# Kernel tuning notes

Hardware: AMD Instinct MI355X
Metric: run time of the kernel (lower is better)

The kernel has to match this reference:

```python
import jax, jax.numpy as jnp
import numpy as np

CHUNK_SIZE = 2048
LOCAL_WINDOW = 384
CHUNK_LEN = CHUNK_SIZE - LOCAL_WINDOW  # 1664
N_HEADS = 16
N_KV_HEADS = 4
HEAD_DIM = 128
HIDDEN = 2048
SEQ = 3 * CHUNK_LEN  # 4992
NEG_INF = -1e9


def _cos_sin(positions, dim=HEAD_DIM, base=10000.0):
    inv = 1.0 / (base ** (np.arange(0, dim, 2, dtype=np.float64) / dim))
    freqs = np.outer(np.asarray(positions, np.float64), inv)
    emb = np.concatenate([freqs, freqs], axis=-1)
    return jnp.asarray(np.cos(emb), jnp.float32), jnp.asarray(np.sin(emb), jnp.float32)


def setup_inputs() -> dict:
    key = jax.random.key(0)
    ks = jax.random.split(key, 5)
    hidden_states = jax.random.normal(ks[0], (1, SEQ, HIDDEN), jnp.float32) * 0.02
    position_ids = jnp.arange(SEQ, dtype=jnp.int32)[None, :]
    q_cos, q_sin = _cos_sin(np.arange(SEQ))                 # intra rotary (positions mod chunk_len)
    qc_cos, qc_sin = _cos_sin(np.arange(SEQ) + CHUNK_LEN)   # cross-chunk rotary variant
    k_cos, k_sin = _cos_sin(np.arange(SEQ))                 # key rotary (absolute positions)
    kv_dim = N_KV_HEADS * HEAD_DIM
    Wq = jax.random.normal(ks[1], (N_HEADS * HEAD_DIM, HIDDEN), jnp.float32) * 0.02
    Wk = jax.random.normal(ks[2], (kv_dim, HIDDEN), jnp.float32) * 0.02
    Wv = jax.random.normal(ks[3], (kv_dim, HIDDEN), jnp.float32) * 0.02
    Wo = jax.random.normal(ks[4], (HIDDEN, N_HEADS * HEAD_DIM), jnp.float32) * 0.02
    return dict(hidden_states=hidden_states, position_ids=position_ids,
                q_cos=q_cos, q_sin=q_sin, qc_cos=qc_cos, qc_sin=qc_sin,
                k_cos=k_cos, k_sin=k_sin, Wq=Wq, Wk=Wk, Wv=Wv, Wo=Wo)


def _rotate_half(x):
    x1, x2 = jnp.split(x, 2, axis=-1)
    return jnp.concatenate([-x2, x1], axis=-1)


def _rope(x, cos_t, sin_t, pid):
    # x: [b,h,s,d], pid: [b,s] -> cos/sin [b,1,s,d]
    cos = cos_t[pid][:, None]
    sin = sin_t[pid][:, None]
    return x * cos + _rotate_half(x) * sin


def _attn(q, k, v, causal):
    # flash-attn semantics: scale = head_dim**-0.5, returns output and fp32 LSE [b,h,q]
    scale = q.shape[-1] ** -0.5
    s = jnp.einsum('bhqd,bhkd->bhqk', q, k).astype(jnp.float32) * scale
    if causal:
        L, K = s.shape[-2], s.shape[-1]
        mask = jnp.tril(jnp.ones((L, K), bool))
        s = jnp.where(mask, s, NEG_INF)
    lse = jax.nn.logsumexp(s, axis=-1)
    p = jax.nn.softmax(s, axis=-1).astype(q.dtype)
    out = jnp.einsum('bhqk,bhkd->bhqd', p, v)
    return out, lse


def _merge(parts):
    # LSE-weighted merge of partial attention outputs (weights detached, as in torch)
    outs = jnp.stack([p[0] for p in parts])       # [n,b,h,q,d]
    lses = jnp.stack([p[1] for p in parts])       # [n,b,h,q] fp32
    w = jax.lax.stop_gradient(jax.nn.softmax(lses, axis=0))
    return jnp.sum(outs * w[..., None].astype(outs.dtype), axis=0)


def _forward(hidden_states, position_ids, q_cos, q_sin, qc_cos, qc_sin, k_cos, k_sin, Wq, Wk, Wv, Wo):
    b, s, _ = hidden_states.shape
    q = (hidden_states @ Wq.T).reshape(b, s, N_HEADS, HEAD_DIM).transpose(0, 2, 1, 3)
    k = (hidden_states @ Wk.T).reshape(b, s, N_KV_HEADS, HEAD_DIM).transpose(0, 2, 1, 3)
    v = (hidden_states @ Wv.T).reshape(b, s, N_KV_HEADS, HEAD_DIM).transpose(0, 2, 1, 3)

    k = _rope(k, k_cos, k_sin, position_ids)
    pid = position_ids % CHUNK_LEN

    groups = N_HEADS // N_KV_HEADS
    k = jnp.repeat(k, groups, axis=1)
    v = jnp.repeat(v, groups, axis=1)

    n_chunks = s // CHUNK_LEN
    # chunk 0: intra causal only
    q0 = _rope(q[:, :, :CHUNK_LEN], q_cos, q_sin, pid[:, :CHUNK_LEN])
    out0, _ = _attn(q0, k[:, :, :CHUNK_LEN], v[:, :, :CHUNK_LEN], causal=True)
    outs = [out0]
    for i in range(1, n_chunks):
        b0 = i * CHUNK_LEN
        e = b0 + CHUNK_LEN
        qi = q[:, :, b0:e]
        pid_c = pid[:, b0:e]
        parts = [_attn(_rope(qi, q_cos, q_sin, pid_c), k[:, :, b0:e], v[:, :, b0:e], causal=True),
                 _attn(_rope(qi, qc_cos, qc_sin, pid_c), k[:, :, b0 - CHUNK_LEN:b0], v[:, :, b0 - CHUNK_LEN:b0], causal=False)]
        if b0 - CHUNK_LEN > 0:
            pid_i = jnp.full_like(pid_c, CHUNK_LEN - 1)
            parts.append(_attn(_rope(qi, qc_cos, qc_sin, pid_i), k[:, :, :b0 - CHUNK_LEN], v[:, :, :b0 - CHUNK_LEN], causal=False))
        outs.append(_merge(parts))
    attn_out = jnp.concatenate(outs, axis=2)                      # [b,h,s,d]
    attn_out = attn_out.transpose(0, 2, 1, 3).reshape(b, s, -1)   # [b,s,h*d]
    return attn_out @ Wo.T


def reference(hidden_states, position_ids, q_cos, q_sin, qc_cos, qc_sin, k_cos, k_sin, Wq, Wk, Wv, Wo):
    return _forward(hidden_states, position_ids, q_cos, q_sin, qc_cos, qc_sin, k_cos, k_sin, Wq, Wk, Wv, Wo)
```

## Files before the change

### kernel.cpp

```cpp
#include <hip/hip_runtime.h>

typedef unsigned short u16;
typedef unsigned int u32;
typedef __attribute__((ext_vector_type(8))) __bf16 bf16x8;
typedef __attribute__((ext_vector_type(4))) float f32x4;
typedef __attribute__((ext_vector_type(16))) float f32x16;

#define CLEN 1664
#define SEQL 4992
#define NHEADS 16
#define HD 128
#define HID 2048
#define KVD 512
#define SCALE 0.08838834764831845f
#define SCLOG2E 0.12752615142058843f

__device__ __forceinline__ u16 f2bf(float f) {
  union { float f; u32 u; } v; v.f = f;
  u32 u = v.u;
  return (u16)((u + 0x7FFFu + ((u >> 16) & 1u)) >> 16);
}
__device__ __forceinline__ float bf2f(u16 h) {
  union { u32 u; float f; } v; v.u = (u32)h << 16;
  return v.f;
}
__device__ __forceinline__ f32x4 mfma16(bf16x8 a, bf16x8 b, f32x4 c) {
  return __builtin_amdgcn_mfma_f32_16x16x32_bf16(a, b, c, 0, 0, 0);
}
__device__ __forceinline__ f32x16 mfma32(bf16x8 a, bf16x8 b, f32x16 c) {
  return __builtin_amdgcn_mfma_f32_32x32x16_bf16(a, b, c, 0, 0, 0);
}
__device__ __forceinline__ u32 cvtpk(float lo, float hi) {
  u32 r;
  asm("v_cvt_pk_bf16_f32 %0, %1, %2" : "=v"(r) : "v"(lo), "v"(hi));
  return r;
}
__device__ __forceinline__ float exp2v(float x) {
  float r;
  asm("v_exp_f32 %0, %1" : "=v"(r) : "v"(x));
  return r;
}
__device__ __forceinline__ void gload_lds16(const u16* g, u16* l) {
  __builtin_amdgcn_global_load_lds((const __attribute__((address_space(1))) void*)g,
                                   (__attribute__((address_space(3))) void*)l, 16, 0, 0);
}

#define CVT_Q0 2555904
#define CVT_Q1 1048576
#define CVT_Q2 262144
#define CVT_Q3 262144
#define CVT_Q4 1048576
__device__ __forceinline__ void cvt4(const float* s, u16* d, int q) {
  float4 v = *(const float4*)(s + (size_t)q * 4);
  uint2 p;
  p.x = (u32)f2bf(v.x) | ((u32)f2bf(v.y) << 16);
  p.y = (u32)f2bf(v.z) | ((u32)f2bf(v.w) << 16);
  *(uint2*)(d + (size_t)q * 4) = p;
}
__global__ void cvt_all_kernel(const float* __restrict__ hidden, const float* __restrict__ Wq,
                               const float* __restrict__ Wk, const float* __restrict__ Wv,
                               const float* __restrict__ Wo, u16* __restrict__ h_bf,
                               u16* __restrict__ Wqkv, u16* __restrict__ Wo_bf) {
  int q = blockIdx.x * blockDim.x + threadIdx.x;
  if (q < CVT_Q0) { cvt4(hidden, h_bf, q); return; }
  q -= CVT_Q0;
  if (q < CVT_Q1) { cvt4(Wq, Wqkv, q); return; }
  q -= CVT_Q1;
  if (q < CVT_Q2) { cvt4(Wk, Wqkv + 2048 * 2048, q); return; }
  q -= CVT_Q2;
  if (q < CVT_Q3) { cvt4(Wv, Wqkv + 2560 * 2048, q); return; }
  q -= CVT_Q3;
  if (q < CVT_Q4) cvt4(Wo, Wo_bf, q);
}

#define RP_N0 1277952
#define RP_N1 851968
#define RP_N2 425984
#define RP_N3 319488
__device__ __forceinline__ void rope8(const u16* __restrict__ src, u16* __restrict__ dst,
                                      const float* __restrict__ ctab, const float* __restrict__ stab,
                                      int s, int dstrow, int col, int rowlen, int pid, float scl) {
  const int dh = col & 127;
  const bool hih = dh >= 64;
  const u16* rowp = src + (size_t)s * rowlen;
  union { uint4 u; u16 h[8]; } X, P, O;
  X.u = *(const uint4*)(rowp + col);
  P.u = *(const uint4*)(rowp + col + (hih ? -64 : 64));
  const float* cp = ctab + pid * 128 + dh;
  const float* sp = stab + pid * 128 + dh;
#pragma unroll
  for (int j = 0; j < 8; ++j) {
    float v = bf2f(X.h[j]) * cp[j] + (hih ? bf2f(P.h[j]) : -bf2f(P.h[j])) * sp[j];
    O.h[j] = f2bf(v * scl);
  }
  *(uint4*)(dst + (size_t)dstrow * rowlen + col) = O.u;
}
__global__ void rope_all_kernel(const u16* __restrict__ q_tmp, const u16* __restrict__ k_tmp,
                                u16* __restrict__ qa, u16* __restrict__ qb, u16* __restrict__ qf,
                                u16* __restrict__ k_bf, const float* __restrict__ q_cos,
                                const float* __restrict__ q_sin, const float* __restrict__ qc_cos,
                                const float* __restrict__ qc_sin, const float* __restrict__ k_cos,
                                const float* __restrict__ k_sin) {
  int o = blockIdx.x * blockDim.x + threadIdx.x;
  if (o < RP_N0) {
    int r = o >> 8, col = (o & 255) * 8;
    rope8(q_tmp, qa, q_cos, q_sin, r, r, col, 2048, r % CLEN, SCLOG2E);
    return;
  }
  o -= RP_N0;
  if (o < RP_N1) {
    int r = o >> 8, col = (o & 255) * 8, s = CLEN + r;
    rope8(q_tmp, qb, qc_cos, qc_sin, s, r, col, 2048, s % CLEN, SCLOG2E);
    return;
  }
  o -= RP_N1;
  if (o < RP_N2) {
    int r = o >> 8, col = (o & 255) * 8, s = 2 * CLEN + r;
    rope8(q_tmp, qf, qc_cos, qc_sin, s, r, col, 2048, CLEN - 1, SCLOG2E);
    return;
  }
  o -= RP_N2;
  if (o < RP_N3) {
    int r = o >> 6, col = (o & 63) * 8;
    rope8(k_tmp, k_bf, k_cos, k_sin, r, r, col, 512, r, 1.0f);
  }
}

__global__ __launch_bounds__(256) void gemm_qkv(const u16* __restrict__ A, const u16* __restrict__ B,
                                                u16* __restrict__ q_tmp, u16* __restrict__ k_tmp,
                                                u16* __restrict__ vT) {
  __shared__ __align__(16) u16 Al[128 * 64];
  __shared__ __align__(16) u16 Bl[128 * 64];
  const int K = HID;
  const int t = threadIdx.x;
  const int lane = t & 63, wid = t >> 6;
  const int g = lane >> 4, c = lane & 15;
  const int wr = wid >> 1, wc = wid & 1;
  const int bid = blockIdx.x;
  const int wg = (bid & 7) * 117 + (bid >> 3);
  const int m0 = (wg % 39) * 128, n0 = (wg / 39) * 128;

  f32x4 acc[4][4];
#pragma unroll
  for (int m = 0; m < 4; ++m)
#pragma unroll
    for (int n = 0; n < 4; ++n) acc[m][n] = (f32x4){0.f, 0.f, 0.f, 0.f};

  const int scol = (t & 7) * 8;
  for (int k0 = 0; k0 < K; k0 += 64) {
    __syncthreads();
#pragma unroll
    for (int i = 0; i < 4; ++i) {
      const int r = i * 32 + (t >> 3);
      gload_lds16(A + (size_t)(m0 + r) * K + k0 + scol, Al + i * 2048 + wid * 512);
      gload_lds16(B + (size_t)(n0 + r) * K + k0 + scol, Bl + i * 2048 + wid * 512);
    }
    __syncthreads();
#pragma unroll
    for (int kk = 0; kk < 2; ++kk) {
      bf16x8 af[4], bfr[4];
#pragma unroll
      for (int m = 0; m < 4; ++m)
        af[m] = *(const bf16x8*)(Al + (wr * 64 + m * 16 + c) * 64 + kk * 32 + g * 8);
#pragma unroll
      for (int n = 0; n < 4; ++n)
        bfr[n] = *(const bf16x8*)(Bl + (wc * 64 + n * 16 + c) * 64 + kk * 32 + g * 8);
#pragma unroll
      for (int m = 0; m < 4; ++m)
#pragma unroll
        for (int n = 0; n < 4; ++n)
          acc[m][n] = mfma16(af[m], bfr[n], acc[m][n]);
    }
  }
#pragma unroll
  for (int m = 0; m < 4; ++m)
#pragma unroll
    for (int n = 0; n < 4; ++n)
#pragma unroll
      for (int j = 0; j < 4; ++j) {
        const int row = m0 + wr * 64 + m * 16 + 4 * g + j;
        const int col = n0 + wc * 64 + n * 16 + c;
        const float v = acc[m][n][j];
        if (n0 < 2048)       q_tmp[(size_t)row * 2048 + col] = f2bf(v);
        else if (n0 < 2560)  k_tmp[(size_t)row * 512 + (col - 2048)] = f2bf(v);
        else                 vT[(size_t)(col - 2560) * SEQL + row] = f2bf(v);
      }
}

__global__ __launch_bounds__(256) void gemm_o(const u16* __restrict__ A, const u16* __restrict__ B,
                                              float* __restrict__ Cf) {
  __shared__ __align__(16) u16 Al[128 * 64];
  __shared__ __align__(16) u16 Bl[128 * 64];
  const int K = HID, N = HID;
  const int t = threadIdx.x;
  const int lane = t & 63, wid = t >> 6;
  const int g = lane >> 4, c = lane & 15;
  const int wr = wid >> 1, wc = wid & 1;
  const int bid = blockIdx.x;
  const int wg = (bid & 7) * 78 + (bid >> 3);
  const int m0 = (wg % 39) * 128, n0 = (wg / 39) * 128;

  f32x4 acc[4][4];
#pragma unroll
  for (int m = 0; m < 4; ++m)
#pragma unroll
    for (int n = 0; n < 4; ++n) acc[m][n] = (f32x4){0.f, 0.f, 0.f, 0.f};

  const int scol = (t & 7) * 8;
  for (int k0 = 0; k0 < K; k0 += 64) {
    __syncthreads();
#pragma unroll
    for (int i = 0; i < 4; ++i) {
      const int r = i * 32 + (t >> 3);
      gload_lds16(A + (size_t)(m0 + r) * K + k0 + scol, Al + i * 2048 + wid * 512);
      gload_lds16(B + (size_t)(n0 + r) * K + k0 + scol, Bl + i * 2048 + wid * 512);
    }
    __syncthreads();
#pragma unroll
    for (int kk = 0; kk < 2; ++kk) {
      bf16x8 af[4], bfr[4];
#pragma unroll
      for (int m = 0; m < 4; ++m)
        af[m] = *(const bf16x8*)(Al + (wr * 64 + m * 16 + c) * 64 + kk * 32 + g * 8);
#pragma unroll
      for (int n = 0; n < 4; ++n)
        bfr[n] = *(const bf16x8*)(Bl + (wc * 64 + n * 16 + c) * 64 + kk * 32 + g * 8);
#pragma unroll
      for (int m = 0; m < 4; ++m)
#pragma unroll
        for (int n = 0; n < 4; ++n)
          acc[m][n] = mfma16(af[m], bfr[n], acc[m][n]);
    }
  }
#pragma unroll
  for (int m = 0; m < 4; ++m)
#pragma unroll
    for (int n = 0; n < 4; ++n)
#pragma unroll
      for (int j = 0; j < 4; ++j) {
        const int row = m0 + wr * 64 + m * 16 + 4 * g + j;
        const int col = n0 + wc * 64 + n * 16 + c;
        Cf[(size_t)row * N + col] = acc[m][n][j];
      }
}

__global__ __launch_bounds__(512, 4) void attn_kernel(
    const u16* __restrict__ qa, const u16* __restrict__ qbuf, const u16* __restrict__ qf,
    const u16* __restrict__ kbf, const u16* __restrict__ vT,
    u16* __restrict__ Opart, float* __restrict__ lseout) {
  __shared__ __align__(16) u16 smem[2 * 16384];

  const int t = threadIdx.x, wid = t >> 6, lane = t & 63;
  const int ql = lane & 31, hi = lane >> 5;
  const int ksr = t >> 4, ksc = t & 15;
  const int vsr = t >> 3, vsc = t & 7;

  const int b = blockIdx.x;
  const int x = b & 7;
  const int j = b >> 3;
  const int k = x >> 1;
  int chunk, seg, qb, head_lo;
  if ((x & 1) == 0) {
    if (j < 56) {
      chunk = (j < 28) ? 1 : 2; seg = 0;
      const int jj = j % 28;
      qb = jj >> 2; head_lo = jj & 3;
    } else {
      const int jj = j - 56;
      chunk = 0; seg = 0;
      qb = 6 - (jj >> 2); head_lo = jj & 3;
    }
  } else {
    if (j < 28) {
      chunk = 2; seg = 1;
      qb = j >> 2; head_lo = j & 3;
    } else if (j < 56) {
      const int jj = j - 28;
      chunk = 1; seg = 1;
      qb = 6 - (jj >> 2); head_lo = jj & 3;
    } else {
      const int jj = j - 56;
      chunk = 2; seg = 2;
      qb = 6 - (jj >> 2); head_lo = jj & 3;
    }
  }
  const int head = k * 4 + head_lo;
  const bool causal = (seg == chunk);
  const int nt = causal ? ((qb == 6) ? 26 : (4 * qb + 4)) : 26;
  const int slot = causal ? 0 : ((chunk - seg == 1) ? 1 : 2);
  const int kvh = k;
  const int kvbase = seg * CLEN;
  const int qcb = qb * 256 + wid * 32;
  const int qpos = qcb + ql;
  const bool wact = qcb < CLEN;

  const u16* qp; int qoff;
  if (causal)                { qp = qa;   qoff = 0; }
  else if (chunk - seg == 1) { qp = qbuf; qoff = CLEN; }
  else                       { qp = qf;   qoff = 2 * CLEN; }

  bf16x8 aq[8];
  {
    const int qrow = wact ? (chunk * CLEN + qpos - qoff) : 0;
    const u16* qptr = qp + (size_t)qrow * HID + head * HD + hi * 8;
#pragma unroll
    for (int ck = 0; ck < 8; ++ck) aq[ck] = *(const bf16x8*)(qptr + ck * 16);
  }

  float l_r = 0.f;
  f32x16 oacc[4];
#pragma unroll
  for (int db = 0; db < 4; ++db)
#pragma unroll
    for (int r = 0; r < 16; ++r) oacc[db][r] = 0.f;

  auto stage = [&](int bb, int kt) {
    const int kv0 = kt * 64;
#pragma unroll
    for (int i = 0; i < 2; ++i) {
      const int rr = ksr + 32 * i;
      const int gs = ksc ^ (rr & 7);
      gload_lds16(kbf + (size_t)(kvbase + kv0 + rr) * KVD + kvh * HD + gs * 8,
                  smem + bb * 16384 + i * 4096 + wid * 512);
    }
#pragma unroll
    for (int i = 0; i < 2; ++i) {
      const int rr = vsr + 64 * i;
      const int gs = vsc ^ (rr & 7);
      gload_lds16(vT + (size_t)(kvh * HD + rr) * SEQL + kvbase + kv0 + gs * 8,
                  smem + bb * 16384 + 8192 + i * 4096 + wid * 512);
    }
  };

  stage(0, 0);
  int cur = 0;
  for (int kt = 0; kt < nt; ++kt) {
    if (kt + 1 < nt) {
      stage(cur ^ 1, kt + 1);
      asm volatile("s_waitcnt vmcnt(4)" ::: "memory");
    } else {
      asm volatile("s_waitcnt vmcnt(0)" ::: "memory");
    }
    __builtin_amdgcn_s_barrier();
    const int kv0 = kt * 64;
    const u16* Kb = smem + cur * 16384;
    const u16* Vb = smem + cur * 16384 + 8192;
#pragma unroll
    for (int s = 0; s < 2; ++s) {
      if (wact && !(causal && kv0 + 32 * s > qcb + 31)) {
        f32x16 sacc;
#pragma unroll
        for (int r = 0; r < 16; ++r) sacc[r] = 0.f;
        const int kr = 32 * s + ql;
        const int r7 = lane & 7;
        __builtin_amdgcn_s_setprio(1);
#pragma unroll
        for (int ck = 0; ck < 8; ++ck) {
          bf16x8 kb = *(const bf16x8*)(Kb + kr * 128 + (((2 * ck + hi) ^ r7) * 8));
          sacc = mfma32(kb, aq[ck], sacc);
        }
        __builtin_amdgcn_s_setprio(0);
        const int thr = qpos - kv0 - 32 * s - 4 * hi;
        float e[16];
        float rs = 0.f;
#pragma unroll
        for (int r = 0; r < 16; ++r) {
          const int crow_r = (r & 3) + 8 * (r >> 2);
          float ev = (causal && crow_r > thr) ? -1e30f : sacc[r];
          e[r] = exp2v(ev);
          rs += e[r];
        }
        rs += __shfl_xor(rs, 32);
        l_r += rs;
        u32 wp[8];
#pragma unroll
        for (int j2 = 0; j2 < 8; ++j2) wp[j2] = cvtpk(e[2 * j2], e[2 * j2 + 1]);
        __builtin_amdgcn_s_setprio(1);
#pragma unroll
        for (int ks = 0; ks < 2; ++ks) {
          union { uint4 u; bf16x8 v; } pa;
          pa.u.x = wp[4 * ks]; pa.u.y = wp[4 * ks + 1];
          pa.u.z = wp[4 * ks + 2]; pa.u.w = wp[4 * ks + 3];
          const int g4a = 8 * s + 4 * ks + hi;
          const int sw = (lane & 7) << 1;
#pragma unroll
          for (int db = 0; db < 4; ++db) {
            const int vrow = 32 * db + ql;
            const uint2 v0 = *(const uint2*)(Vb + vrow * 64 + ((g4a ^ sw) * 4));
            const uint2 v1 = *(const uint2*)(Vb + vrow * 64 + (((g4a + 2) ^ sw) * 4));
            union { uint4 u; bf16x8 v; } bv;
            bv.u.x = v0.x; bv.u.y = v0.y; bv.u.z = v1.x; bv.u.w = v1.y;
            oacc[db] = mfma32(pa.v, bv.v, oacc[db]);
          }
        }
        __builtin_amdgcn_s_setprio(0);
      }
    }
    __builtin_amdgcn_s_barrier();
    cur ^= 1;
  }
  if (wact) {
    const float linv = 1.0f / l_r;
    u16* scr = smem + wid * 4096;
#pragma unroll
    for (int r = 0; r < 16; ++r) {
      const int rrow = (r & 3) + 8 * (r >> 2) + 4 * hi;
      const float li = __shfl(linv, rrow);
#pragma unroll
      for (int db = 0; db < 4; ++db)
        scr[rrow * 128 + db * 32 + ql] = f2bf(oacc[db][r] * li);
    }
    asm volatile("s_waitcnt lgkmcnt(0)" ::: "memory");
    const int rcol = lane & 15;
#pragma unroll
    for (int p = 0; p < 8; ++p) {
      const int row = p * 4 + (lane >> 4);
      uint4 v = *(const uint4*)(scr + row * 128 + rcol * 8);
      const size_t grow = (size_t)(chunk * CLEN + qcb + row);
      *(uint4*)(Opart + ((size_t)slot * SEQL + grow) * HID + head * HD + rcol * 8) = v;
    }
    if (hi == 0)
      lseout[((size_t)slot * NHEADS + head) * SEQL + chunk * CLEN + qcb + ql] = __logf(l_r);
  }
}

__global__ void merge_kernel(const u16* __restrict__ Opart, const float* __restrict__ lse,
                             u16* __restrict__ amrg) {
  const int idx = blockIdx.x * blockDim.x + threadIdx.x;
  const int row = idx >> 8;
  const int col = (idx & 255) * 8;
  const int head = col >> 7;
  const int np = row / CLEN + 1;
  float ls[3];
  float mx = -1e30f;
  for (int i = 0; i < np; ++i) {
    ls[i] = lse[((size_t)i * NHEADS + head) * SEQL + row];
    mx = fmaxf(mx, ls[i]);
  }
  float wsum = 0.f;
  for (int i = 0; i < np; ++i) { ls[i] = __expf(ls[i] - mx); wsum += ls[i]; }
  const float inv = 1.0f / wsum;
  float acc[8];
#pragma unroll
  for (int j = 0; j < 8; ++j) acc[j] = 0.f;
  for (int i = 0; i < np; ++i) {
    union { uint4 u; u16 h[8]; } X;
    X.u = *(const uint4*)(Opart + ((size_t)i * SEQL + row) * (size_t)HID + col);
#pragma unroll
    for (int j = 0; j < 8; ++j) acc[j] += ls[i] * bf2f(X.h[j]);
  }
  union { uint4 u; u16 h[8]; } O;
#pragma unroll
  for (int j = 0; j < 8; ++j) O.h[j] = f2bf(acc[j] * inv);
  *(uint4*)(amrg + (size_t)row * 2048 + col) = O.u;
}

extern "C" void kernel_launch(void* const* d_in, const int* in_sizes, int n_in,
                              void* d_out, int out_size, void* d_ws, size_t ws_size,
                              hipStream_t stream) {
  (void)in_sizes; (void)n_in; (void)out_size; (void)ws_size;
  const float* hidden = (const float*)d_in[0];
  const float* q_cos = (const float*)d_in[2];
  const float* q_sin = (const float*)d_in[3];
  const float* qc_cos = (const float*)d_in[4];
  const float* qc_sin = (const float*)d_in[5];
  const float* k_cos = (const float*)d_in[6];
  const float* k_sin = (const float*)d_in[7];
  const float* Wq = (const float*)d_in[8];
  const float* Wk = (const float*)d_in[9];
  const float* Wv = (const float*)d_in[10];
  const float* Wo = (const float*)d_in[11];
  float* out = (float*)d_out;

  char* ws = (char*)d_ws;
  u16* Wo_bf = (u16*)(ws + 0);
  u16* qa    = (u16*)(ws + 8388608);
  u16* qb    = (u16*)(ws + 28835840);
  u16* qf    = (u16*)(ws + 42467328);
  u16* k_bf  = (u16*)(ws + 49283072);
  u16* vT    = (u16*)(ws + 54394880);
  char* BIG  = ws + 59506688;
  u16* h_bf  = (u16*)(BIG + 0);
  u16* Wqkv  = (u16*)(BIG + 20447232);
  u16* q_tmp = (u16*)(BIG + 33030144);
  u16* k_tmp = (u16*)(BIG + 53477376);
  u16* Opart = (u16*)(BIG + 0);
  float* lse = (float*)(BIG + 61341696);
  u16* amrg  = qa;

  cvt_all_kernel<<<dim3(20224), dim3(256), 0, stream>>>(hidden, Wq, Wk, Wv, Wo, h_bf, Wqkv, Wo_bf);
  gemm_qkv<<<dim3(936), 256, 0, stream>>>(h_bf, Wqkv, q_tmp, k_tmp, vT);
  rope_all_kernel<<<dim3(11232), dim3(256), 0, stream>>>(q_tmp, k_tmp, qa, qb, qf, k_bf,
                                                         q_cos, q_sin, qc_cos, qc_sin, k_cos, k_sin);
  attn_kernel<<<dim3(672), dim3(512), 0, stream>>>(qa, qb, qf, k_bf, vT, Opart, lse);
  merge_kernel<<<dim3(SEQL), dim3(256), 0, stream>>>(Opart, lse, amrg);
  gemm_o<<<dim3(624), 256, 0, stream>>>(amrg, Wo_bf, out);
}
```

Measured before the change: 507.2 us.

## Load K/V directly from global memory per wave instead of shared-memory staging

Replaces the block-wide double-buffered LDS staging of K and V tiles, and the barriers around it, with per-wave direct global loads into registers. Each wave now iterates only over its own causal range, so there is no block synchronisation and the launch-bounds occupancy hint is dropped. The aim is to remove barrier stalls and idle waves in causal blocks. The cost is that the 8 waves no longer share K/V loads through LDS, so global/L2 traffic rises, V loads become small strided 8-byte accesses, and no prefetch hides load latency.

```diff
diff --git a/kernel.cpp b/kernel.cpp
--- a/kernel.cpp
+++ b/kernel.cpp
@@ -244,16 +244,14 @@
       }
 }
 
-__global__ __launch_bounds__(512, 4) void attn_kernel(
+__global__ __launch_bounds__(512) void attn_kernel(
     const u16* __restrict__ qa, const u16* __restrict__ qbuf, const u16* __restrict__ qf,
     const u16* __restrict__ kbf, const u16* __restrict__ vT,
     u16* __restrict__ Opart, float* __restrict__ lseout) {
-  __shared__ __align__(16) u16 smem[2 * 16384];
+  __shared__ __align__(16) u16 scr_all[8 * 4096];
 
   const int t = threadIdx.x, wid = t >> 6, lane = t & 63;
   const int ql = lane & 31, hi = lane >> 5;
-  const int ksr = t >> 4, ksc = t & 15;
-  const int vsr = t >> 3, vsc = t & 7;
 
   const int b = blockIdx.x;
   const int x = b & 7;
@@ -286,13 +284,13 @@
   }
   const int head = k * 4 + head_lo;
   const bool causal = (seg == chunk);
-  const int nt = causal ? ((qb == 6) ? 26 : (4 * qb + 4)) : 26;
   const int slot = causal ? 0 : ((chunk - seg == 1) ? 1 : 2);
   const int kvh = k;
   const int kvbase = seg * CLEN;
   const int qcb = qb * 256 + wid * 32;
   const int qpos = qcb + ql;
   const bool wact = qcb < CLEN;
+  const int ntw = wact ? (causal ? ((qcb >> 6) + 1) : 26) : 0;
 
   const u16* qp; int qoff;
   if (causal)                { qp = qa;   qoff = 0; }
@@ -314,94 +312,64 @@
 #pragma unroll
     for (int r = 0; r < 16; ++r) oacc[db][r] = 0.f;
 
-  auto stage = [&](int bb, int kt) {
+  const u16* kbase = kbf + (size_t)kvbase * KVD + kvh * HD;
+  const u16* vbase = vT + (size_t)(kvh * HD) * SEQL + kvbase;
+
+  for (int kt = 0; kt < ntw; ++kt) {
     const int kv0 = kt * 64;
 #pragma unroll
-    for (int i = 0; i < 2; ++i) {
-      const int rr = ksr + 32 * i;
-      const int gs = ksc ^ (rr & 7);
-      gload_lds16(kbf + (size_t)(kvbase + kv0 + rr) * KVD + kvh * HD + gs * 8,
-                  smem + bb * 16384 + i * 4096 + wid * 512);
-    }
-#pragma unroll
-    for (int i = 0; i < 2; ++i) {
-      const int rr = vsr + 64 * i;
-      const int gs = vsc ^ (rr & 7);
-      gload_lds16(vT + (size_t)(kvh * HD + rr) * SEQL + kvbase + kv0 + gs * 8,
-                  smem + bb * 16384 + 8192 + i * 4096 + wid * 512);
-    }
-  };
-
-  stage(0, 0);
-  int cur = 0;
-  for (int kt = 0; kt < nt; ++kt) {
-    if (kt + 1 < nt) {
-      stage(cur ^ 1, kt + 1);
-      asm volatile("s_waitcnt vmcnt(4)" ::: "memory");
-    } else {
-      asm volatile("s_waitcnt vmcnt(0)" ::: "memory");
-    }
-    __builtin_amdgcn_s_barrier();
-    const int kv0 = kt * 64;
-    const u16* Kb = smem + cur * 16384;
-    const u16* Vb = smem + cur * 16384 + 8192;
-#pragma unroll
     for (int s = 0; s < 2; ++s) {
-      if (wact && !(causal && kv0 + 32 * s > qcb + 31)) {
-        f32x16 sacc;
-#pragma unroll
-        for (int r = 0; r < 16; ++r) sacc[r] = 0.f;
-        const int kr = 32 * s + ql;
-        const int r7 = lane & 7;
-        __builtin_amdgcn_s_setprio(1);
-#pragma unroll
-        for (int ck = 0; ck < 8; ++ck) {
-          bf16x8 kb = *(const bf16x8*)(Kb + kr * 128 + (((2 * ck + hi) ^ r7) * 8));
-          sacc = mfma32(kb, aq[ck], sacc);
+      if (causal && kv0 + 32 * s > qcb + 31) break;
+      const u16* krow = kbase + (size_t)(kv0 + 32 * s + ql) * KVD;
+      bf16x8 kb[8];
+#pragma unroll
+      for (int ck = 0; ck < 8; ++ck)
+        kb[ck] = *(const bf16x8*)(krow + (2 * ck + hi) * 8);
+      f32x16 sacc;
+#pragma unroll
+      for (int r = 0; r < 16; ++r) sacc[r] = 0.f;
+      __builtin_amdgcn_s_setprio(1);
+#pragma unroll
+      for (int ck = 0; ck < 8; ++ck) sacc = mfma32(kb[ck], aq[ck], sacc);
+      __builtin_amdgcn_s_setprio(0);
+      const int thr = qpos - kv0 - 32 * s - 4 * hi;
+      float e[16];
+      float rs = 0.f;
+#pragma unroll
+      for (int r = 0; r < 16; ++r) {
+        const int crow_r = (r & 3) + 8 * (r >> 2);
+        float ev = (causal && crow_r > thr) ? -1e30f : sacc[r];
+        e[r] = exp2v(ev);
+        rs += e[r];
+      }
+      rs += __shfl_xor(rs, 32);
+      l_r += rs;
+      u32 wp[8];
+#pragma unroll
+      for (int j2 = 0; j2 < 8; ++j2) wp[j2] = cvtpk(e[2 * j2], e[2 * j2 + 1]);
+      __builtin_amdgcn_s_setprio(1);
+#pragma unroll
+      for (int ks = 0; ks < 2; ++ks) {
+        union { uint4 u; bf16x8 v; } pa;
+        pa.u.x = wp[4 * ks]; pa.u.y = wp[4 * ks + 1];
+        pa.u.z = wp[4 * ks + 2]; pa.u.w = wp[4 * ks + 3];
+        const int g4a = 8 * s + 4 * ks + hi;
+#pragma unroll
+        for (int db = 0; db < 4; ++db) {
+          const u16* vrowp = vbase + (size_t)(32 * db + ql) * SEQL + kv0;
+          const uint2 v0 = *(const uint2*)(vrowp + g4a * 4);
+          const uint2 v1 = *(const uint2*)(vrowp + g4a * 4 + 8);
+          union { uint4 u; bf16x8 v; } bv;
+          bv.u.x = v0.x; bv.u.y = v0.y; bv.u.z = v1.x; bv.u.w = v1.y;
+          oacc[db] = mfma32(pa.v, bv.v, oacc[db]);
         }
-        __builtin_amdgcn_s_setprio(0);
-        const int thr = qpos - kv0 - 32 * s - 4 * hi;
-        float e[16];
-        float rs = 0.f;
-#pragma unroll
-        for (int r = 0; r < 16; ++r) {
-          const int crow_r = (r & 3) + 8 * (r >> 2);
-          float ev = (causal && crow_r > thr) ? -1e30f : sacc[r];
-          e[r] = exp2v(ev);
-          rs += e[r];
-        }
-        rs += __shfl_xor(rs, 32);
-        l_r += rs;
-        u32 wp[8];
-#pragma unroll
-        for (int j2 = 0; j2 < 8; ++j2) wp[j2] = cvtpk(e[2 * j2], e[2 * j2 + 1]);
-        __builtin_amdgcn_s_setprio(1);
-#pragma unroll
-        for (int ks = 0; ks < 2; ++ks) {
-          union { uint4 u; bf16x8 v; } pa;
-          pa.u.x = wp[4 * ks]; pa.u.y = wp[4 * ks + 1];
-          pa.u.z = wp[4 * ks + 2]; pa.u.w = wp[4 * ks + 3];
-          const int g4a = 8 * s + 4 * ks + hi;
-          const int sw = (lane & 7) << 1;
-#pragma unroll
-          for (int db = 0; db < 4; ++db) {
-            const int vrow = 32 * db + ql;
-            const uint2 v0 = *(const uint2*)(Vb + vrow * 64 + ((g4a ^ sw) * 4));
-            const uint2 v1 = *(const uint2*)(Vb + vrow * 64 + (((g4a + 2) ^ sw) * 4));
-            union { uint4 u; bf16x8 v; } bv;
-            bv.u.x = v0.x; bv.u.y = v0.y; bv.u.z = v1.x; bv.u.w = v1.y;
-            oacc[db] = mfma32(pa.v, bv.v, oacc[db]);
-          }
-        }
-        __builtin_amdgcn_s_setprio(0);
       }
-    }
-    __builtin_amdgcn_s_barrier();
-    cur ^= 1;
+      __builtin_amdgcn_s_setprio(0);
+    }
   }
   if (wact) {
     const float linv = 1.0f / l_r;
-    u16* scr = smem + wid * 4096;
+    u16* scr = scr_all + wid * 4096;
 #pragma unroll
     for (int r = 0; r < 16; ++r) {
       const int rrow = (r & 3) + 8 * (r >> 2) + 4 * hi;
```

Measured after the change: 875.0 us. 1.73x slower.
